# Performance work log

Measured on AMD Instinct MI355X. Metric: run time of the kernel, lower is better.

## Reference

```python
import jax, jax.numpy as jnp
import numpy as np

N_NODES = 100000
N_EDGES = 1600000
H_FEATS = 64


def setup_inputs() -> dict:
    key = jax.random.key(0)
    k_h, k_src, k_dst, k_w1, k_b1, k_w2, k_b2 = jax.random.split(key, 7)
    h = jax.random.normal(k_h, (N_NODES, H_FEATS), dtype=jnp.float32)
    src = jax.random.randint(k_src, (N_EDGES,), 0, N_NODES, dtype=jnp.int64)
    dst = jax.random.randint(k_dst, (N_EDGES,), 0, N_NODES, dtype=jnp.int64)
    # Linear params (torch Linear: y = x @ W.T + b). Store as [in, out] for jnp.
    lim1 = 1.0 / np.sqrt(2 * H_FEATS)
    W1 = jax.random.uniform(k_w1, (2 * H_FEATS, H_FEATS), minval=-lim1, maxval=lim1, dtype=jnp.float32)
    b1 = jax.random.uniform(k_b1, (H_FEATS,), minval=-lim1, maxval=lim1, dtype=jnp.float32)
    lim2 = 1.0 / np.sqrt(H_FEATS)
    W2 = jax.random.uniform(k_w2, (H_FEATS, 1), minval=-lim2, maxval=lim2, dtype=jnp.float32)
    b2 = jax.random.uniform(k_b2, (1,), minval=-lim2, maxval=lim2, dtype=jnp.float32)
    return {"h": h, "src": src, "dst": dst, "W1": W1, "b1": b1, "W2": W2, "b2": b2}


def reference(h, src, dst, W1, b1, W2, b2):
    # Gather src/dst node features per edge, avoid materializing the concat by
    # splitting W1 into the src-half and dst-half of the contraction.
    W1s, W1d = W1[:H_FEATS], W1[H_FEATS:]            # each [h, h]
    h_src = h[src]                                    # [E, h]
    h_dst = h[dst]                                    # [E, h]
    hidden = jax.nn.relu(h_src @ W1s + h_dst @ W1d + b1)  # [E, h]
    score = (hidden @ W2 + b2)[:, 0]                  # [E]
    return score
```

## Files before the change

kernel.cpp:

```cpp
#include <hip/hip_runtime.h>
#include <hip/hip_fp16.h>


#define HF    64
#define PITCH 144
#define TPB   2

typedef __attribute__((ext_vector_type(8))) short bf16x8;
typedef __attribute__((ext_vector_type(4))) float f32x4;

__device__ __forceinline__ short f2bf(float x) {
    unsigned u = __builtin_bit_cast(unsigned, x);
    unsigned r = (u + 0x7fffu + ((u >> 16) & 1u)) >> 16;
    return (short)r;
}

__device__ __forceinline__ unsigned char q8(float v, float inv) {
    return (unsigned char)(int)rintf(fmaf(v, inv, 127.0f));
}

__global__ __launch_bounds__(256) void node_proj_kernel(
    const float* __restrict__ h, const float* __restrict__ W1,
    const float* __restrict__ b1, unsigned char* __restrict__ P8,
    unsigned char* __restrict__ Q8, float* __restrict__ Psc,
    float* __restrict__ Qsc, int n_nodes)
{
    __shared__ unsigned char eb8[64 * PITCH];
    __shared__ float pscl[64];
    __shared__ float qscl[64];

    const int tid  = threadIdx.x;
    const int wave = tid >> 6;
    const int lane = tid & 63;
    const int q    = lane >> 4;
    const int n    = lane & 15;

    bf16x8 bfrag[8][2];
    #pragma unroll
    for (int t = 0; t < 8; ++t) {
        const float* wb = W1 + ((t >= 4) ? HF * HF : 0) + (t & 3) * 16 + n;
        #pragma unroll
        for (int kb = 0; kb < 2; ++kb) {
            #pragma unroll
            for (int j = 0; j < 8; ++j)
                bfrag[t][kb][j] = f2bf(wb[(kb * 32 + q * 8 + j) * HF]);
        }
    }
    const float bias_n  = b1[0 * 16 + n];
    const float bias_n1 = b1[1 * 16 + n];
    const float bias_n2 = b1[2 * 16 + n];
    const float bias_n3 = b1[3 * 16 + n];

    for (int it = 0; it < TPB; ++it) {
        const int tile = blockIdx.x * TPB + it;
        const int n0   = tile * 64;
        if (n0 >= n_nodes) break;
        const int nrow = (n_nodes - n0 < 64) ? (n_nodes - n0) : 64;

        bf16x8 a0, a1;
        {
            int row = n0 + wave * 16 + n;
            if (row >= n_nodes) row = n_nodes - 1;
            const float* hr = h + (size_t)row * HF + q * 8;
            const float4 u0 = *(const float4*)(hr);
            const float4 u1 = *(const float4*)(hr + 4);
            const float4 v0 = *(const float4*)(hr + 32);
            const float4 v1 = *(const float4*)(hr + 36);
            a0[0] = f2bf(u0.x); a0[1] = f2bf(u0.y); a0[2] = f2bf(u0.z); a0[3] = f2bf(u0.w);
            a0[4] = f2bf(u1.x); a0[5] = f2bf(u1.y); a0[6] = f2bf(u1.z); a0[7] = f2bf(u1.w);
            a1[0] = f2bf(v0.x); a1[1] = f2bf(v0.y); a1[2] = f2bf(v0.z); a1[3] = f2bf(v0.w);
            a1[4] = f2bf(v1.x); a1[5] = f2bf(v1.y); a1[6] = f2bf(v1.z); a1[7] = f2bf(v1.w);
        }

        f32x4 acc[8];
        #pragma unroll
        for (int t = 0; t < 8; ++t) {
            acc[t] = (f32x4){0.f, 0.f, 0.f, 0.f};
            acc[t] = __builtin_amdgcn_mfma_f32_16x16x32_bf16(a0, bfrag[t][0], acc[t], 0, 0, 0);
            acc[t] = __builtin_amdgcn_mfma_f32_16x16x32_bf16(a1, bfrag[t][1], acc[t], 0, 0, 0);
        }

        if (it > 0) __syncthreads();

        #pragma unroll
        for (int r = 0; r < 4; ++r) {
            const int row = wave * 16 + q * 4 + r;
            const float p0 = acc[0][r] + bias_n;
            const float p1 = acc[1][r] + bias_n1;
            const float p2 = acc[2][r] + bias_n2;
            const float p3 = acc[3][r] + bias_n3;
            const float q0 = acc[4][r], q1 = acc[5][r];
            const float q2 = acc[6][r], q3 = acc[7][r];

            float pa = fmaxf(fmaxf(__builtin_fabsf(p0), __builtin_fabsf(p1)),
                             fmaxf(__builtin_fabsf(p2), __builtin_fabsf(p3)));
            float qa = fmaxf(fmaxf(__builtin_fabsf(q0), __builtin_fabsf(q1)),
                             fmaxf(__builtin_fabsf(q2), __builtin_fabsf(q3)));
            #pragma unroll
            for (int m = 1; m < 16; m <<= 1) {
                pa = fmaxf(pa, __shfl_xor(pa, m, 16));
                qa = fmaxf(qa, __shfl_xor(qa, m, 16));
            }
            pa = fmaxf(pa, 1e-12f);
            qa = fmaxf(qa, 1e-12f);
            const float pinv = 127.0f / pa;
            const float qinv = 127.0f / qa;

            unsigned char* er = eb8 + row * PITCH;
            er[ 0 + n]      = q8(p0, pinv);
            er[16 + n]      = q8(p1, pinv);
            er[32 + n]      = q8(p2, pinv);
            er[48 + n]      = q8(p3, pinv);
            er[64 +  0 + n] = q8(q0, qinv);
            er[64 + 16 + n] = q8(q1, qinv);
            er[64 + 32 + n] = q8(q2, qinv);
            er[64 + 48 + n] = q8(q3, qinv);
            if (n == 0) {
                pscl[row] = pa * (1.0f / 127.0f);
                qscl[row] = qa * (1.0f / 127.0f);
            }
        }
        __syncthreads();

        #pragma unroll
        for (int s = 0; s < 2; ++s) {
            const int idx  = tid + s * 256;
            const int row  = idx >> 3;
            const int part = idx & 7;
            if (row < nrow) {
                const uint4 v = *(const uint4*)&eb8[row * PITCH + part * 16];
                unsigned char* dstp = (part < 4)
                    ? (P8 + (size_t)(n0 + row) * HF + part * 16)
                    : (Q8 + (size_t)(n0 + row) * HF + (part - 4) * 16);
                *(uint4*)dstp = v;
            }
        }
        if (tid < 128) {
            const int rr = tid & 63;
            if (rr < nrow) {
                if (tid < 64) Psc[n0 + rr] = pscl[rr];
                else          Qsc[n0 + rr] = qscl[rr];
            }
        }
    }
}

__device__ __forceinline__ float dot8q(uint2 pv, uint2 qv, float4 wa, float4 wb,
                                       float ps, float qs) {
    const float C = -127.0f * (ps + qs);
    float acc = 0.f;
    {
        const unsigned u = pv.x, v = qv.x;
        float x;
        x = fmaf((float)(u & 255u),         ps, fmaf((float)(v & 255u),         qs, C));
        acc = fmaf(fmaxf(x, 0.f), wa.x, acc);
        x = fmaf((float)((u >> 8) & 255u),  ps, fmaf((float)((v >> 8) & 255u),  qs, C));
        acc = fmaf(fmaxf(x, 0.f), wa.y, acc);
        x = fmaf((float)((u >> 16) & 255u), ps, fmaf((float)((v >> 16) & 255u), qs, C));
        acc = fmaf(fmaxf(x, 0.f), wa.z, acc);
        x = fmaf((float)(u >> 24),          ps, fmaf((float)(v >> 24),          qs, C));
        acc = fmaf(fmaxf(x, 0.f), wa.w, acc);
    }
    {
        const unsigned u = pv.y, v = qv.y;
        float x;
        x = fmaf((float)(u & 255u),         ps, fmaf((float)(v & 255u),         qs, C));
        acc = fmaf(fmaxf(x, 0.f), wb.x, acc);
        x = fmaf((float)((u >> 8) & 255u),  ps, fmaf((float)((v >> 8) & 255u),  qs, C));
        acc = fmaf(fmaxf(x, 0.f), wb.y, acc);
        x = fmaf((float)((u >> 16) & 255u), ps, fmaf((float)((v >> 16) & 255u), qs, C));
        acc = fmaf(fmaxf(x, 0.f), wb.z, acc);
        x = fmaf((float)(u >> 24),          ps, fmaf((float)(v >> 24),          qs, C));
        acc = fmaf(fmaxf(x, 0.f), wb.w, acc);
    }
    return acc;
}

__device__ __forceinline__ float red8(float v) {
    v += __shfl_xor(v, 4, 8);
    v += __shfl_xor(v, 2, 8);
    v += __shfl_xor(v, 1, 8);
    return v;
}

__global__ __launch_bounds__(256) void edge_score_kernel(
    const unsigned char* __restrict__ P8, const unsigned char* __restrict__ Q8,
    const float* __restrict__ Psc, const float* __restrict__ Qsc,
    const int* __restrict__ src, const int* __restrict__ dst,
    const float* __restrict__ W2, const float* __restrict__ b2,
    float* __restrict__ out, int n_edges)
{
    const int tid   = blockIdx.x * 256 + threadIdx.x;
    const int sub   = threadIdx.x & 7;
    const int group = tid >> 3;
    const int j0    = sub * 8;
    const int e0    = group * 8;
    if (e0 >= n_edges) return;

    const float4 w2a = *(const float4*)(W2 + j0);
    const float4 w2b = *(const float4*)(W2 + j0 + 4);
    const float bias2 = b2[0];

    if (e0 + 8 <= n_edges) {
        const int4 sA = *(const int4*)(src + e0);
        const int4 sB = *(const int4*)(src + e0 + 4);
        const int4 dA = *(const int4*)(dst + e0);
        const int4 dB = *(const int4*)(dst + e0 + 4);

        const float ps_own = Psc[src[e0 + sub]];
        const float qs_own = Qsc[dst[e0 + sub]];

        const uint2 p0 = *(const uint2*)(P8 + (size_t)sA.x * HF + j0);
        const uint2 p1 = *(const uint2*)(P8 + (size_t)sA.y * HF + j0);
        const uint2 p2 = *(const uint2*)(P8 + (size_t)sA.z * HF + j0);
        const uint2 p3 = *(const uint2*)(P8 + (size_t)sA.w * HF + j0);
        const uint2 p4 = *(const uint2*)(P8 + (size_t)sB.x * HF + j0);
        const uint2 p5 = *(const uint2*)(P8 + (size_t)sB.y * HF + j0);
        const uint2 p6 = *(const uint2*)(P8 + (size_t)sB.z * HF + j0);
        const uint2 p7 = *(const uint2*)(P8 + (size_t)sB.w * HF + j0);
        const uint2 q0 = *(const uint2*)(Q8 + (size_t)dA.x * HF + j0);
        const uint2 q1 = *(const uint2*)(Q8 + (size_t)dA.y * HF + j0);
        const uint2 q2 = *(const uint2*)(Q8 + (size_t)dA.z * HF + j0);
        const uint2 q3 = *(const uint2*)(Q8 + (size_t)dA.w * HF + j0);
        const uint2 q4 = *(const uint2*)(Q8 + (size_t)dB.x * HF + j0);
        const uint2 q5 = *(const uint2*)(Q8 + (size_t)dB.y * HF + j0);
        const uint2 q6 = *(const uint2*)(Q8 + (size_t)dB.z * HF + j0);
        const uint2 q7 = *(const uint2*)(Q8 + (size_t)dB.w * HF + j0);

        float s0 = red8(dot8q(p0, q0, w2a, w2b, __shfl(ps_own, 0, 8), __shfl(qs_own, 0, 8)));
        float s1 = red8(dot8q(p1, q1, w2a, w2b, __shfl(ps_own, 1, 8), __shfl(qs_own, 1, 8)));
        float s2 = red8(dot8q(p2, q2, w2a, w2b, __shfl(ps_own, 2, 8), __shfl(qs_own, 2, 8)));
        float s3 = red8(dot8q(p3, q3, w2a, w2b, __shfl(ps_own, 3, 8), __shfl(qs_own, 3, 8)));
        float s4 = red8(dot8q(p4, q4, w2a, w2b, __shfl(ps_own, 4, 8), __shfl(qs_own, 4, 8)));
        float s5 = red8(dot8q(p5, q5, w2a, w2b, __shfl(ps_own, 5, 8), __shfl(qs_own, 5, 8)));
        float s6 = red8(dot8q(p6, q6, w2a, w2b, __shfl(ps_own, 6, 8), __shfl(qs_own, 6, 8)));
        float s7 = red8(dot8q(p7, q7, w2a, w2b, __shfl(ps_own, 7, 8), __shfl(qs_own, 7, 8)));

        if (sub == 0) {
            *(float4*)(out + e0)     = make_float4(s0 + bias2, s1 + bias2,
                                                   s2 + bias2, s3 + bias2);
            *(float4*)(out + e0 + 4) = make_float4(s4 + bias2, s5 + bias2,
                                                   s6 + bias2, s7 + bias2);
        }
    } else {
        for (int e = e0; e < n_edges; ++e) {
            const int s = src[e];
            const int d = dst[e];
            const float ps = Psc[s];
            const float qs = Qsc[d];
            const uint2 pv = *(const uint2*)(P8 + (size_t)s * HF + j0);
            const uint2 qv = *(const uint2*)(Q8 + (size_t)d * HF + j0);
            float sc = red8(dot8q(pv, qv, w2a, w2b, ps, qs));
            if (sub == 0) out[e] = sc + bias2;
        }
    }
}

extern "C" void kernel_launch(void* const* d_in, const int* in_sizes, int n_in,
                              void* d_out, int out_size, void* d_ws, size_t ws_size,
                              hipStream_t stream) {
    const float* h   = (const float*)d_in[0];
    const int*   src = (const int*)d_in[1];
    const int*   dst = (const int*)d_in[2];
    const float* W1  = (const float*)d_in[3];
    const float* b1  = (const float*)d_in[4];
    const float* W2  = (const float*)d_in[5];
    const float* b2  = (const float*)d_in[6];
    float* out = (float*)d_out;

    const int n_nodes = in_sizes[0] / HF;
    const int n_edges = in_sizes[1];

    unsigned char* P8 = (unsigned char*)d_ws;
    unsigned char* Q8 = P8 + (size_t)n_nodes * HF;
    float* Psc = (float*)(Q8 + (size_t)n_nodes * HF);
    float* Qsc = Psc + n_nodes;

    const int ntiles   = (n_nodes + 63) / 64;
    const int nblocks1 = (ntiles + TPB - 1) / TPB;
    node_proj_kernel<<<nblocks1, 256, 0, stream>>>(h, W1, b1, P8, Q8, Psc, Qsc, n_nodes);

    const int ngroups  = (n_edges + 7) / 8;
    const int nblocks2 = (ngroups + 31) / 32;
    edge_score_kernel<<<nblocks2, 256, 0, stream>>>(P8, Q8, Psc, Qsc, src, dst, W2, b2, out, n_edges);
}
```

Measured before the change: 147.8 us.

## Bucket edges by src/dst node range for locality-aware gather

Adds a scatter pass that sorts edges into 128 buckets keyed on coarse src and dst node ranges. Each record packs the edge id and both node ids into 64 bits, and a bucketed edge kernel then gathers quantized node projections, so each block touches a small slice of P8/Q8 that can stay in L2/MALL. Block ids are swizzled across XCDs, and the per-node scales are interleaved into a single float2 array. The price is extra launches, an atomic histogram, a 12.8MB record write and read, and scattered output writes. Edges are dropped if a bucket overflows its fixed capacity.

```diff
diff --git a/kernel.cpp b/kernel.cpp
--- a/kernel.cpp
+++ b/kernel.cpp
@@ -5,6 +5,8 @@
 #define HF    64
 #define PITCH 144
 #define TPB   2
+#define NBUCK 128
+#define EPB   1024
 
 typedef __attribute__((ext_vector_type(8))) short bf16x8;
 typedef __attribute__((ext_vector_type(4))) float f32x4;
@@ -22,8 +24,7 @@
 __global__ __launch_bounds__(256) void node_proj_kernel(
     const float* __restrict__ h, const float* __restrict__ W1,
     const float* __restrict__ b1, unsigned char* __restrict__ P8,
-    unsigned char* __restrict__ Q8, float* __restrict__ Psc,
-    float* __restrict__ Qsc, int n_nodes)
+    unsigned char* __restrict__ Q8, float* __restrict__ S, int n_nodes)
 {
     __shared__ unsigned char eb8[64 * PITCH];
     __shared__ float pscl[64];
@@ -135,11 +136,61 @@
                 *(uint4*)dstp = v;
             }
         }
-        if (tid < 128) {
-            const int rr = tid & 63;
-            if (rr < nrow) {
-                if (tid < 64) Psc[n0 + rr] = pscl[rr];
-                else          Qsc[n0 + rr] = qscl[rr];
+        if (tid < nrow) {
+            *(float2*)(S + 2 * (size_t)(n0 + tid)) =
+                make_float2(pscl[tid], qscl[tid]);
+        }
+    }
+}
+
+__global__ void zero_counters_kernel(unsigned int* __restrict__ counters) {
+    counters[threadIdx.x] = 0u;
+}
+
+#define SCAT_EPT 16
+__global__ __launch_bounds__(256) void bucket_scatter_kernel(
+    const int* __restrict__ src, const int* __restrict__ dst,
+    unsigned long long* __restrict__ recs, unsigned int* __restrict__ counters,
+    int n_edges, int cap, float invs, float invd)
+{
+    __shared__ unsigned int hist[NBUCK];
+    __shared__ unsigned int gbase[NBUCK];
+    __shared__ unsigned int rank[NBUCK];
+    const int tid = threadIdx.x;
+    if (tid < NBUCK) { hist[tid] = 0; rank[tid] = 0; }
+    __syncthreads();
+
+    const int blockbase = blockIdx.x * (256 * SCAT_EPT);
+    int sv[SCAT_EPT], dv[SCAT_EPT], bk[SCAT_EPT];
+    #pragma unroll
+    for (int i = 0; i < SCAT_EPT; ++i) {
+        const int e = blockbase + i * 256 + tid;
+        int s_ = 0, d_ = 0, b = -1;
+        if (e < n_edges) {
+            s_ = src[e];
+            d_ = dst[e];
+            const int bs = min(7,  (int)((float)s_ * invs));
+            const int bd = min(15, (int)((float)d_ * invd));
+            b = bs * 16 + bd;
+            atomicAdd(&hist[b], 1u);
+        }
+        sv[i] = s_; dv[i] = d_; bk[i] = b;
+    }
+    __syncthreads();
+    if (tid < NBUCK) gbase[tid] = atomicAdd(&counters[tid], hist[tid]);
+    __syncthreads();
+    #pragma unroll
+    for (int i = 0; i < SCAT_EPT; ++i) {
+        const int b = bk[i];
+        if (b >= 0) {
+            const int e = blockbase + i * 256 + tid;
+            const unsigned r = atomicAdd(&rank[b], 1u);
+            const unsigned slot = gbase[b] + r;
+            if (slot < (unsigned)cap) {
+                recs[(size_t)b * cap + slot] =
+                      (unsigned long long)(unsigned)e
+                    | ((unsigned long long)(unsigned)sv[i] << 21)
+                    | ((unsigned long long)(unsigned)dv[i] << 38);
             }
         }
     }
@@ -183,9 +234,71 @@
     return v;
 }
 
+__global__ __launch_bounds__(256) void bucket_edge_kernel(
+    const unsigned char* __restrict__ P8, const unsigned char* __restrict__ Q8,
+    const float* __restrict__ S, const unsigned long long* __restrict__ recs,
+    const unsigned int* __restrict__ counters,
+    const float* __restrict__ W2, const float* __restrict__ b2,
+    float* __restrict__ out, int cap, int bpb, int nblk)
+{
+    const int bid = blockIdx.x;
+    int swz = bid;
+    if ((nblk & 7) == 0) {
+        const int cpx = nblk >> 3;
+        swz = (bid & 7) * cpx + (bid >> 3);
+    }
+    const int bucket = swz / bpb;
+    const int chunk  = swz - bucket * bpb;
+    const int cnt  = min((int)counters[bucket], cap);
+    const int s0   = chunk * EPB;
+    if (s0 >= cnt) return;
+    const size_t base = (size_t)bucket * cap;
+
+    const int tid = threadIdx.x;
+    const int sub = tid & 7;
+    const int g   = tid >> 3;
+    const int j0  = sub * 8;
+    const float4 w2a = *(const float4*)(W2 + j0);
+    const float4 w2b = *(const float4*)(W2 + j0 + 4);
+    const float bias2 = b2[0];
+
+    #pragma unroll 1
+    for (int it = 0; it < EPB / 256; ++it) {
+        const int e8 = s0 + it * 256 + g * 8;
+        if (e8 >= cnt) break;
+        const int slot = e8 + sub;
+        unsigned long long rec = 0;
+        if (slot < cnt) rec = recs[base + slot];
+        const int eid = (int)(rec & 0x1FFFFFu);
+        const int sn  = (int)((rec >> 21) & 0x1FFFFu);
+        const int dn  = (int)(rec >> 38);
+        const float ps_own = S[2 * sn];
+        const float qs_own = S[2 * dn + 1];
+
+        uint2 p[8], q[8];
+        #pragma unroll
+        for (int j = 0; j < 8; ++j) {
+            const int snj = __shfl(sn, j, 8);
+            const int dnj = __shfl(dn, j, 8);
+            p[j] = *(const uint2*)(P8 + (size_t)snj * HF + j0);
+            q[j] = *(const uint2*)(Q8 + (size_t)dnj * HF + j0);
+        }
+        float sc[8];
+        #pragma unroll
+        for (int j = 0; j < 8; ++j) {
+            sc[j] = red8(dot8q(p[j], q[j], w2a, w2b,
+                               __shfl(ps_own, j, 8), __shfl(qs_own, j, 8)));
+        }
+        float my = sc[0];
+        #pragma unroll
+        for (int j = 1; j < 8; ++j) my = (sub == j) ? sc[j] : my;
+        if (slot < cnt) out[eid] = my + bias2;
+    }
+}
+
 __global__ __launch_bounds__(256) void edge_score_kernel(
     const unsigned char* __restrict__ P8, const unsigned char* __restrict__ Q8,
-    const float* __restrict__ Psc, const float* __restrict__ Qsc,
+    const float* __restrict__ S,
     const int* __restrict__ src, const int* __restrict__ dst,
     const float* __restrict__ W2, const float* __restrict__ b2,
     float* __restrict__ out, int n_edges)
@@ -206,25 +319,24 @@
         const int4 sB = *(const int4*)(src + e0 + 4);
         const int4 dA = *(const int4*)(dst + e0);
         const int4 dB = *(const int4*)(dst + e0 + 4);
-
-        const float ps_own = Psc[src[e0 + sub]];
-        const float qs_own = Qsc[dst[e0 + sub]];
+        const float ps_own = S[2 * src[e0 + sub]];
+        const float qs_own = S[2 * dst[e0 + sub] + 1];
 
         const uint2 p0 = *(const uint2*)(P8 + (size_t)sA.x * HF + j0);
+        const uint2 q0 = *(const uint2*)(Q8 + (size_t)dA.x * HF + j0);
         const uint2 p1 = *(const uint2*)(P8 + (size_t)sA.y * HF + j0);
+        const uint2 q1 = *(const uint2*)(Q8 + (size_t)dA.y * HF + j0);
         const uint2 p2 = *(const uint2*)(P8 + (size_t)sA.z * HF + j0);
+        const uint2 q2 = *(const uint2*)(Q8 + (size_t)dA.z * HF + j0);
         const uint2 p3 = *(const uint2*)(P8 + (size_t)sA.w * HF + j0);
+        const uint2 q3 = *(const uint2*)(Q8 + (size_t)dA.w * HF + j0);
         const uint2 p4 = *(const uint2*)(P8 + (size_t)sB.x * HF + j0);
+        const uint2 q4 = *(const uint2*)(Q8 + (size_t)dB.x * HF + j0);
         const uint2 p5 = *(const uint2*)(P8 + (size_t)sB.y * HF + j0);
+        const uint2 q5 = *(const uint2*)(Q8 + (size_t)dB.y * HF + j0);
         const uint2 p6 = *(const uint2*)(P8 + (size_t)sB.z * HF + j0);
+        const uint2 q6 = *(const uint2*)(Q8 + (size_t)dB.z * HF + j0);
         const uint2 p7 = *(const uint2*)(P8 + (size_t)sB.w * HF + j0);
-        const uint2 q0 = *(const uint2*)(Q8 + (size_t)dA.x * HF + j0);
-        const uint2 q1 = *(const uint2*)(Q8 + (size_t)dA.y * HF + j0);
-        const uint2 q2 = *(const uint2*)(Q8 + (size_t)dA.z * HF + j0);
-        const uint2 q3 = *(const uint2*)(Q8 + (size_t)dA.w * HF + j0);
-        const uint2 q4 = *(const uint2*)(Q8 + (size_t)dB.x * HF + j0);
-        const uint2 q5 = *(const uint2*)(Q8 + (size_t)dB.y * HF + j0);
-        const uint2 q6 = *(const uint2*)(Q8 + (size_t)dB.z * HF + j0);
         const uint2 q7 = *(const uint2*)(Q8 + (size_t)dB.w * HF + j0);
 
         float s0 = red8(dot8q(p0, q0, w2a, w2b, __shfl(ps_own, 0, 8), __shfl(qs_own, 0, 8)));
@@ -246,8 +358,8 @@
         for (int e = e0; e < n_edges; ++e) {
             const int s = src[e];
             const int d = dst[e];
-            const float ps = Psc[s];
-            const float qs = Qsc[d];
+            const float ps = S[2 * s];
+            const float qs = S[2 * d + 1];
             const uint2 pv = *(const uint2*)(P8 + (size_t)s * HF + j0);
             const uint2 qv = *(const uint2*)(Q8 + (size_t)d * HF + j0);
             float sc = red8(dot8q(pv, qv, w2a, w2b, ps, qs));
@@ -273,14 +385,35 @@
 
     unsigned char* P8 = (unsigned char*)d_ws;
     unsigned char* Q8 = P8 + (size_t)n_nodes * HF;
-    float* Psc = (float*)(Q8 + (size_t)n_nodes * HF);
-    float* Qsc = Psc + n_nodes;
-
-    const int ntiles   = (n_nodes + 63) / 64;
-    const int nblocks1 = (ntiles + TPB - 1) / TPB;
-    node_proj_kernel<<<nblocks1, 256, 0, stream>>>(h, W1, b1, P8, Q8, Psc, Qsc, n_nodes);
-
-    const int ngroups  = (n_edges + 7) / 8;
-    const int nblocks2 = (ngroups + 31) / 32;
-    edge_score_kernel<<<nblocks2, 256, 0, stream>>>(P8, Q8, Psc, Qsc, src, dst, W2, b2, out, n_edges);
-}
+    float* S = (float*)(Q8 + (size_t)n_nodes * HF);
+    unsigned int* counters = (unsigned int*)(S + 2 * (size_t)n_nodes);
+    unsigned long long* recs = (unsigned long long*)
+        (((uintptr_t)(counters + NBUCK) + 7) & ~(uintptr_t)7);
+
+    int cap = (n_edges / NBUCK + n_edges / (NBUCK * 8) + 256 + EPB - 1) / EPB * EPB;
+    if (cap < EPB) cap = EPB;
+    const size_t need = (size_t)((char*)(recs + (size_t)NBUCK * cap) - (char*)d_ws);
+    const bool bucketed = (need <= ws_size) &&
+                          (n_edges < (1 << 21)) && (n_nodes < (1 << 17));
+
+    const int ntiles = (n_nodes + 63) / 64;
+    const int nb1 = (ntiles + TPB - 1) / TPB;
+    node_proj_kernel<<<nb1, 256, 0, stream>>>(h, W1, b1, P8, Q8, S, n_nodes);
+
+    if (bucketed) {
+        zero_counters_kernel<<<1, NBUCK, 0, stream>>>(counters);
+        const int sblocks = (n_edges + 256 * SCAT_EPT - 1) / (256 * SCAT_EPT);
+        bucket_scatter_kernel<<<sblocks, 256, 0, stream>>>(
+            src, dst, recs, counters, n_edges, cap,
+            8.0f / (float)n_nodes, 16.0f / (float)n_nodes);
+        const int bpb  = cap / EPB;
+        const int nblk = NBUCK * bpb;
+        bucket_edge_kernel<<<nblk, 256, 0, stream>>>(
+            P8, Q8, S, recs, counters, W2, b2, out, cap, bpb, nblk);
+    } else {
+        const int ngroups = (n_edges + 7) / 8;
+        const int nb2 = (ngroups + 31) / 32;
+        edge_score_kernel<<<nb2, 256, 0, stream>>>(
+            P8, Q8, S, src, dst, W2, b2, out, n_edges);
+    }
+}
```

Measured after the change: 170.3 us. 15.2% more time.

## Embed quantized per-node scale in int8 feature LSBs to drop scale gathers

Applied to the files above, without the earlier changes.

Per-node scales are no longer kept as separate float arrays. Each scale is snapped to a 32-level logarithmic grid, and its 5-bit index is stored in the low bits of the first five quantized bytes of each row. The edge kernel rebuilds the scale from the bytes it already gathers, which removes two random 4-byte gathers per edge and the dependent src/dst index reloads. The cost is lower precision: scales are coarser and five values per row lose their LSB, and scales above 2^3.6 are clamped, which could overflow the int8 range.

```diff
diff --git a/kernel.cpp b/kernel.cpp
--- a/kernel.cpp
+++ b/kernel.cpp
@@ -19,15 +19,21 @@
     return (unsigned char)(int)rintf(fmaf(v, inv, 127.0f));
 }
 
+__device__ __forceinline__ int scale_idx(float amax) {
+    const float lg = __log2f(amax * 4.0f) * 8.0f;
+    int i = (int)ceilf(lg);
+    return (i < 0) ? 0 : (i > 31 ? 31 : i);
+}
+__device__ __forceinline__ float scale_from_idx(int i) {
+    return 0.25f * exp2f((float)i * 0.125f);
+}
+
 __global__ __launch_bounds__(256) void node_proj_kernel(
     const float* __restrict__ h, const float* __restrict__ W1,
     const float* __restrict__ b1, unsigned char* __restrict__ P8,
-    unsigned char* __restrict__ Q8, float* __restrict__ Psc,
-    float* __restrict__ Qsc, int n_nodes)
+    unsigned char* __restrict__ Q8, int n_nodes)
 {
     __shared__ unsigned char eb8[64 * PITCH];
-    __shared__ float pscl[64];
-    __shared__ float qscl[64];
 
     const int tid  = threadIdx.x;
     const int wave = tid >> 6;
@@ -101,24 +107,29 @@
                 pa = fmaxf(pa, __shfl_xor(pa, m, 16));
                 qa = fmaxf(qa, __shfl_xor(qa, m, 16));
             }
-            pa = fmaxf(pa, 1e-12f);
-            qa = fmaxf(qa, 1e-12f);
-            const float pinv = 127.0f / pa;
-            const float qinv = 127.0f / qa;
+            pa = fmaxf(pa, 1e-6f);
+            qa = fmaxf(qa, 1e-6f);
+            const int   ip   = scale_idx(pa);
+            const int   iq   = scale_idx(qa);
+            const float pinv = 127.0f / scale_from_idx(ip);
+            const float qinv = 127.0f / scale_from_idx(iq);
+
+            unsigned char bp0 = q8(p0, pinv);
+            unsigned char bq0 = q8(q0, qinv);
+            if (n < 5) {
+                bp0 = (unsigned char)((bp0 & 0xFEu) | ((ip >> n) & 1));
+                bq0 = (unsigned char)((bq0 & 0xFEu) | ((iq >> n) & 1));
+            }
 
             unsigned char* er = eb8 + row * PITCH;
-            er[ 0 + n]      = q8(p0, pinv);
+            er[ 0 + n]      = bp0;
             er[16 + n]      = q8(p1, pinv);
             er[32 + n]      = q8(p2, pinv);
             er[48 + n]      = q8(p3, pinv);
-            er[64 +  0 + n] = q8(q0, qinv);
+            er[64 +  0 + n] = bq0;
             er[64 + 16 + n] = q8(q1, qinv);
             er[64 + 32 + n] = q8(q2, qinv);
             er[64 + 48 + n] = q8(q3, qinv);
-            if (n == 0) {
-                pscl[row] = pa * (1.0f / 127.0f);
-                qscl[row] = qa * (1.0f / 127.0f);
-            }
         }
         __syncthreads();
 
@@ -135,14 +146,14 @@
                 *(uint4*)dstp = v;
             }
         }
-        if (tid < 128) {
-            const int rr = tid & 63;
-            if (rr < nrow) {
-                if (tid < 64) Psc[n0 + rr] = pscl[rr];
-                else          Qsc[n0 + rr] = qscl[rr];
-            }
-        }
-    }
+    }
+}
+
+__device__ __forceinline__ float dec_scale(uint2 v) {
+    const unsigned x = v.x, y = v.y;
+    const int i = (int)((x & 1u) | ((x >> 7) & 2u) | ((x >> 14) & 4u)
+                      | ((x >> 21) & 8u) | ((y << 4) & 16u));
+    return 0.25f * exp2f((float)i * 0.125f) * (1.0f / 127.0f);
 }
 
 __device__ __forceinline__ float dot8q(uint2 pv, uint2 qv, float4 wa, float4 wb,
@@ -185,7 +196,6 @@
 
 __global__ __launch_bounds__(256) void edge_score_kernel(
     const unsigned char* __restrict__ P8, const unsigned char* __restrict__ Q8,
-    const float* __restrict__ Psc, const float* __restrict__ Qsc,
     const int* __restrict__ src, const int* __restrict__ dst,
     const float* __restrict__ W2, const float* __restrict__ b2,
     float* __restrict__ out, int n_edges)
@@ -207,34 +217,40 @@
         const int4 dA = *(const int4*)(dst + e0);
         const int4 dB = *(const int4*)(dst + e0 + 4);
 
-        const float ps_own = Psc[src[e0 + sub]];
-        const float qs_own = Qsc[dst[e0 + sub]];
-
         const uint2 p0 = *(const uint2*)(P8 + (size_t)sA.x * HF + j0);
+        const uint2 q0 = *(const uint2*)(Q8 + (size_t)dA.x * HF + j0);
         const uint2 p1 = *(const uint2*)(P8 + (size_t)sA.y * HF + j0);
+        const uint2 q1 = *(const uint2*)(Q8 + (size_t)dA.y * HF + j0);
         const uint2 p2 = *(const uint2*)(P8 + (size_t)sA.z * HF + j0);
+        const uint2 q2 = *(const uint2*)(Q8 + (size_t)dA.z * HF + j0);
         const uint2 p3 = *(const uint2*)(P8 + (size_t)sA.w * HF + j0);
+        const uint2 q3 = *(const uint2*)(Q8 + (size_t)dA.w * HF + j0);
         const uint2 p4 = *(const uint2*)(P8 + (size_t)sB.x * HF + j0);
+        const uint2 q4 = *(const uint2*)(Q8 + (size_t)dB.x * HF + j0);
         const uint2 p5 = *(const uint2*)(P8 + (size_t)sB.y * HF + j0);
+        const uint2 q5 = *(const uint2*)(Q8 + (size_t)dB.y * HF + j0);
         const uint2 p6 = *(const uint2*)(P8 + (size_t)sB.z * HF + j0);
+        const uint2 q6 = *(const uint2*)(Q8 + (size_t)dB.z * HF + j0);
         const uint2 p7 = *(const uint2*)(P8 + (size_t)sB.w * HF + j0);
-        const uint2 q0 = *(const uint2*)(Q8 + (size_t)dA.x * HF + j0);
-        const uint2 q1 = *(const uint2*)(Q8 + (size_t)dA.y * HF + j0);
-        const uint2 q2 = *(const uint2*)(Q8 + (size_t)dA.z * HF + j0);
-        const uint2 q3 = *(const uint2*)(Q8 + (size_t)dA.w * HF + j0);
-        const uint2 q4 = *(const uint2*)(Q8 + (size_t)dB.x * HF + j0);
-        const uint2 q5 = *(const uint2*)(Q8 + (size_t)dB.y * HF + j0);
-        const uint2 q6 = *(const uint2*)(Q8 + (size_t)dB.z * HF + j0);
         const uint2 q7 = *(const uint2*)(Q8 + (size_t)dB.w * HF + j0);
 
-        float s0 = red8(dot8q(p0, q0, w2a, w2b, __shfl(ps_own, 0, 8), __shfl(qs_own, 0, 8)));
-        float s1 = red8(dot8q(p1, q1, w2a, w2b, __shfl(ps_own, 1, 8), __shfl(qs_own, 1, 8)));
-        float s2 = red8(dot8q(p2, q2, w2a, w2b, __shfl(ps_own, 2, 8), __shfl(qs_own, 2, 8)));
-        float s3 = red8(dot8q(p3, q3, w2a, w2b, __shfl(ps_own, 3, 8), __shfl(qs_own, 3, 8)));
-        float s4 = red8(dot8q(p4, q4, w2a, w2b, __shfl(ps_own, 4, 8), __shfl(qs_own, 4, 8)));
-        float s5 = red8(dot8q(p5, q5, w2a, w2b, __shfl(ps_own, 5, 8), __shfl(qs_own, 5, 8)));
-        float s6 = red8(dot8q(p6, q6, w2a, w2b, __shfl(ps_own, 6, 8), __shfl(qs_own, 6, 8)));
-        float s7 = red8(dot8q(p7, q7, w2a, w2b, __shfl(ps_own, 7, 8), __shfl(qs_own, 7, 8)));
+        const float ps0 = __shfl(dec_scale(p0), 0, 8), qs0 = __shfl(dec_scale(q0), 0, 8);
+        const float ps1 = __shfl(dec_scale(p1), 0, 8), qs1 = __shfl(dec_scale(q1), 0, 8);
+        const float ps2 = __shfl(dec_scale(p2), 0, 8), qs2 = __shfl(dec_scale(q2), 0, 8);
+        const float ps3 = __shfl(dec_scale(p3), 0, 8), qs3 = __shfl(dec_scale(q3), 0, 8);
+        const float ps4 = __shfl(dec_scale(p4), 0, 8), qs4 = __shfl(dec_scale(q4), 0, 8);
+        const float ps5 = __shfl(dec_scale(p5), 0, 8), qs5 = __shfl(dec_scale(q5), 0, 8);
+        const float ps6 = __shfl(dec_scale(p6), 0, 8), qs6 = __shfl(dec_scale(q6), 0, 8);
+        const float ps7 = __shfl(dec_scale(p7), 0, 8), qs7 = __shfl(dec_scale(q7), 0, 8);
+
+        const float s0 = red8(dot8q(p0, q0, w2a, w2b, ps0, qs0));
+        const float s1 = red8(dot8q(p1, q1, w2a, w2b, ps1, qs1));
+        const float s2 = red8(dot8q(p2, q2, w2a, w2b, ps2, qs2));
+        const float s3 = red8(dot8q(p3, q3, w2a, w2b, ps3, qs3));
+        const float s4 = red8(dot8q(p4, q4, w2a, w2b, ps4, qs4));
+        const float s5 = red8(dot8q(p5, q5, w2a, w2b, ps5, qs5));
+        const float s6 = red8(dot8q(p6, q6, w2a, w2b, ps6, qs6));
+        const float s7 = red8(dot8q(p7, q7, w2a, w2b, ps7, qs7));
 
         if (sub == 0) {
             *(float4*)(out + e0)     = make_float4(s0 + bias2, s1 + bias2,
@@ -246,10 +262,10 @@
         for (int e = e0; e < n_edges; ++e) {
             const int s = src[e];
             const int d = dst[e];
-            const float ps = Psc[s];
-            const float qs = Qsc[d];
             const uint2 pv = *(const uint2*)(P8 + (size_t)s * HF + j0);
             const uint2 qv = *(const uint2*)(Q8 + (size_t)d * HF + j0);
+            const float ps = __shfl(dec_scale(pv), 0, 8);
+            const float qs = __shfl(dec_scale(qv), 0, 8);
             float sc = red8(dot8q(pv, qv, w2a, w2b, ps, qs));
             if (sub == 0) out[e] = sc + bias2;
         }
@@ -273,14 +289,12 @@
 
     unsigned char* P8 = (unsigned char*)d_ws;
     unsigned char* Q8 = P8 + (size_t)n_nodes * HF;
-    float* Psc = (float*)(Q8 + (size_t)n_nodes * HF);
-    float* Qsc = Psc + n_nodes;
-
-    const int ntiles   = (n_nodes + 63) / 64;
-    const int nblocks1 = (ntiles + TPB - 1) / TPB;
-    node_proj_kernel<<<nblocks1, 256, 0, stream>>>(h, W1, b1, P8, Q8, Psc, Qsc, n_nodes);
-
-    const int ngroups  = (n_edges + 7) / 8;
-    const int nblocks2 = (ngroups + 31) / 32;
-    edge_score_kernel<<<nblocks2, 256, 0, stream>>>(P8, Q8, Psc, Qsc, src, dst, W2, b2, out, n_edges);
-}
+
+    const int ntiles = (n_nodes + 63) / 64;
+    const int nb1 = (ntiles + TPB - 1) / TPB;
+    node_proj_kernel<<<nb1, 256, 0, stream>>>(h, W1, b1, P8, Q8, n_nodes);
+
+    const int ngroups = (n_edges + 7) / 8;
+    const int nb2 = (ngroups + 31) / 32;
+    edge_score_kernel<<<nb2, 256, 0, stream>>>(P8, Q8, src, dst, W2, b2, out, n_edges);
+}
```

New measurement: 143.6 us. 1.03x faster.
